# Kernel tuning notes

Measured on AMD Instinct MI355X. Metric: run time of the kernel, lower is better.

## Reference

```python
import jax, jax.numpy as jnp
import numpy as np

VOCAB = 50257
NUM_TAGS = 50
EMB_DIM = 128
CTX = 2
N_TOKENS = 262144


def setup_inputs() -> dict:
    key = jax.random.key(0)
    k1, k2, k3, k4 = jax.random.split(key, 4)
    tokens = jax.random.randint(k1, (N_TOKENS,), 0, VOCAB, dtype=jnp.int64 if jax.config.jax_enable_x64 else jnp.int32)
    emb_table = jax.random.normal(k2, (VOCAB, EMB_DIM), dtype=jnp.float32)
    W = jax.random.normal(k3, (NUM_TAGS, EMB_DIM * (1 + 2 * CTX)), dtype=jnp.float32) * 0.05
    b = jax.random.normal(k4, (NUM_TAGS,), dtype=jnp.float32) * 0.05
    return {"tokens": tokens, "emb_table": emb_table, "W": W, "b": b}


def reference(tokens, emb_table, W, b):
    # [N, D] embedding gather
    emb = emb_table[tokens]
    n = emb.shape[0]
    # zero-pad CTX positions on each side (matches torch.zeros_like padding)
    padded = jnp.pad(emb, ((CTX, CTX), (0, 0)))
    # sliding window concat: [N, (2*CTX+1)*D] via 2*CTX+1 shifted views
    windows = jnp.concatenate([padded[i:i + n] for i in range(2 * CTX + 1)], axis=-1)
    logits = windows @ W.T + b  # [N, num_tags]
    log_probs = jax.nn.log_softmax(logits, axis=-1)
    return log_probs
```

## Files before the change

### kernel.cpp

```cpp
#include <hip/hip_runtime.h>
#include <hip/hip_bf16.h>

#define VOCAB 50257
#define NTAGS 50
#define EMB   128
#define NTOK  262144
#define KD    640
#define WPAD  64

#define TPB   64
#define TOKPB 64
#define ROWS  68

typedef __attribute__((ext_vector_type(4))) float f32x4;
typedef __attribute__((ext_vector_type(8))) short bf16x8;

__device__ __forceinline__ ushort f2bf(float f) {
    union { float f; unsigned u; } v; v.f = f;
    unsigned u = v.u;
    return (ushort)((u + 0x7fffu + ((u >> 16) & 1u)) >> 16);
}

__device__ __forceinline__ void gload_lds16(const void* g, void* l) {
    __builtin_amdgcn_global_load_lds(
        (const __attribute__((address_space(1))) unsigned*)g,
        (__attribute__((address_space(3))) unsigned*)l, 16, 0, 0);
}

__global__ void conv_k(const float* __restrict__ emb, const float* __restrict__ W,
                       ushort* __restrict__ embb, ushort* __restrict__ wb) {
    const int etotal = (VOCAB + 1) * EMB;
    int idx = (blockIdx.x * blockDim.x + threadIdx.x) * 4;
    if (idx < etotal) {
        float4 v = {0.f, 0.f, 0.f, 0.f};
        if (idx < VOCAB * EMB) v = *(const float4*)(emb + idx);
        ushort4 o = { f2bf(v.x), f2bf(v.y), f2bf(v.z), f2bf(v.w) };
        *(ushort4*)(embb + idx) = o;
    } else {
        int wi = idx - etotal;
        if (wi < WPAD * KD) {
            #pragma unroll
            for (int k = 0; k < 4; ++k) {
                int j = wi + k;
                int tag = j / KD;
                wb[j] = f2bf(tag < NTAGS ? W[j] : 0.f);
            }
        }
    }
}

__global__ __launch_bounds__(TPB)
void tagger_k(const int* __restrict__ tokens, const ushort* __restrict__ embb,
              const ushort* __restrict__ Wb, const float* __restrict__ bias,
              float* __restrict__ out) {
    __shared__ ushort smem[ROWS * EMB];

    const int lane = threadIdx.x & 63;
    const int c = lane & 15;
    const int q = lane >> 4;
    const int bb = blockIdx.x * TOKPB;

    {
        const int rsub = lane >> 4;
        const int pc   = lane & 15;
        #pragma unroll
        for (int g = 0; g < 17; ++g) {
            int i = g * 4 + rsub;
            int t = bb - 2 + i;
            int tok = (t >= 0 && t < NTOK) ? tokens[t] : VOCAB;
            int sc = pc ^ (i & 7);
            gload_lds16(embb + (size_t)tok * EMB + sc * 8, (char*)smem + g * 1024);
        }
    }
    __syncthreads();

    f32x4 acc[4][4];
    #pragma unroll
    for (int mt = 0; mt < 4; ++mt)
        #pragma unroll
        for (int nt = 0; nt < 4; ++nt)
            acc[mt][nt] = (f32x4){0.f, 0.f, 0.f, 0.f};

    #pragma unroll
    for (int p = 0; p < 5; ++p) {
        #pragma unroll
        for (int kk = 0; kk < 4; ++kk) {
            bf16x8 a[4], bf[4];
            #pragma unroll
            for (int mt = 0; mt < 4; ++mt) {
                int r  = mt * 16 + c + p;
                int pc = (4 * kk + q) ^ (r & 7);
                a[mt] = *(const bf16x8*)((const char*)smem + r * 256 + pc * 16);
            }
            const int kf = p * 128 + kk * 32 + q * 8;
            #pragma unroll
            for (int nt = 0; nt < 4; ++nt)
                bf[nt] = *(const bf16x8*)(Wb + (nt * 16 + c) * KD + kf);
            __builtin_amdgcn_s_setprio(1);
            #pragma unroll
            for (int mt = 0; mt < 4; ++mt)
                #pragma unroll
                for (int nt = 0; nt < 4; ++nt)
                    acc[mt][nt] = __builtin_amdgcn_mfma_f32_16x16x32_bf16(
                        a[mt], bf[nt], acc[mt][nt], 0, 0, 0);
            __builtin_amdgcn_s_setprio(0);
        }
    }

    float bv[4];
    #pragma unroll
    for (int nt = 0; nt < 4; ++nt) {
        int tag = nt * 16 + c;
        bv[nt] = (tag < NTAGS) ? bias[tag] : 0.f;
    }

    #pragma unroll
    for (int mt = 0; mt < 4; ++mt) {
        #pragma unroll
        for (int j = 0; j < 4; ++j) {
            const int row = bb + mt * 16 + q * 4 + j;
            float v[4];
            float m = -1e30f;
            #pragma unroll
            for (int nt = 0; nt < 4; ++nt) {
                float x = acc[mt][nt][j] + bv[nt];
                v[nt] = x;
                if (nt * 16 + c < NTAGS) m = fmaxf(m, x);
            }
            #pragma unroll
            for (int mask = 8; mask >= 1; mask >>= 1)
                m = fmaxf(m, __shfl_xor(m, mask));
            float s = 0.f;
            #pragma unroll
            for (int nt = 0; nt < 4; ++nt)
                if (nt * 16 + c < NTAGS) s += __expf(v[nt] - m);
            #pragma unroll
            for (int mask = 8; mask >= 1; mask >>= 1)
                s += __shfl_xor(s, mask);
            const float L = m + __logf(s);
            #pragma unroll
            for (int nt = 0; nt < 4; ++nt) {
                int tag = nt * 16 + c;
                if (tag < NTAGS) out[row * NTAGS + tag] = v[nt] - L;
            }
        }
    }
}

extern "C" void kernel_launch(void* const* d_in, const int* in_sizes, int n_in,
                              void* d_out, int out_size, void* d_ws, size_t ws_size,
                              hipStream_t stream) {
    const int*   tokens = (const int*)d_in[0];
    const float* emb    = (const float*)d_in[1];
    const float* W      = (const float*)d_in[2];
    const float* b      = (const float*)d_in[3];
    float* out = (float*)d_out;

    ushort* embb = (ushort*)d_ws;
    ushort* Wb   = embb + (size_t)(VOCAB + 1) * EMB;

    {
        const int etotal = (VOCAB + 1) * EMB;
        const int total4 = (etotal + WPAD * KD) / 4;
        conv_k<<<(total4 + 255) / 256, 256, 0, stream>>>(emb, W, embb, Wb);
    }
    {
        const int nblk = NTOK / TOKPB;
        tagger_k<<<nblk, TPB, 0, stream>>>(tokens, embb, Wb, b, out);
    }
}
```

Baseline: 81.86 us.

## Software-pipeline MFMA loop with register prefetch of W and LDS fragments

Hoists the token index loads, the bias loads and the first W fragment loads ahead of the LDS gather. The k-loop becomes a flat 20-step loop with a 4-deep register ring for W fragments and a 2-deep ring for A fragments, so loads for later steps are issued while the current MFMAs run. Launch bounds now ask for 2 blocks per CU. The extra live registers raise VGPR pressure and could cause spills.

```diff
diff --git a/kernel.cpp b/kernel.cpp
--- a/kernel.cpp
+++ b/kernel.cpp
@@ -11,6 +11,7 @@
 #define TPB   64
 #define TOKPB 64
 #define ROWS  68
+#define STEPS 20
 
 typedef __attribute__((ext_vector_type(4))) float f32x4;
 typedef __attribute__((ext_vector_type(8))) short bf16x8;
@@ -49,7 +50,7 @@
     }
 }
 
-__global__ __launch_bounds__(TPB)
+__global__ __launch_bounds__(TPB, 2)
 void tagger_k(const int* __restrict__ tokens, const ushort* __restrict__ embb,
               const ushort* __restrict__ Wb, const float* __restrict__ bias,
               float* __restrict__ out) {
@@ -59,17 +60,41 @@
     const int c = lane & 15;
     const int q = lane >> 4;
     const int bb = blockIdx.x * TOKPB;
+    const int rsub = lane >> 4;
+
+    int tokid[17];
+    #pragma unroll
+    for (int g = 0; g < 17; ++g) {
+        int t = bb - 2 + g * 4 + rsub;
+        tokid[g] = (t >= 0 && t < NTOK) ? tokens[t] : VOCAB;
+    }
+
+    const ushort* bp[4];
+    #pragma unroll
+    for (int nt = 0; nt < 4; ++nt)
+        bp[nt] = Wb + (nt * 16 + c) * KD + q * 8;
+
+    bf16x8 Bb[4][4];
+    #pragma unroll
+    for (int s = 0; s < 4; ++s)
+        #pragma unroll
+        for (int nt = 0; nt < 4; ++nt)
+            Bb[s][nt] = *(const bf16x8*)(bp[nt] + (s >> 2) * 128 + (s & 3) * 32);
+
+    float bv[4];
+    #pragma unroll
+    for (int nt = 0; nt < 4; ++nt) {
+        int tag = nt * 16 + c;
+        bv[nt] = bias[tag < NTAGS ? tag : NTAGS - 1];
+    }
 
     {
-        const int rsub = lane >> 4;
-        const int pc   = lane & 15;
+        const int pc = lane & 15;
         #pragma unroll
         for (int g = 0; g < 17; ++g) {
             int i = g * 4 + rsub;
-            int t = bb - 2 + i;
-            int tok = (t >= 0 && t < NTOK) ? tokens[t] : VOCAB;
             int sc = pc ^ (i & 7);
-            gload_lds16(embb + (size_t)tok * EMB + sc * 8, (char*)smem + g * 1024);
+            gload_lds16(embb + (size_t)tokid[g] * EMB + sc * 8, (char*)smem + g * 1024);
         }
     }
     __syncthreads();
@@ -81,37 +106,43 @@
         for (int nt = 0; nt < 4; ++nt)
             acc[mt][nt] = (f32x4){0.f, 0.f, 0.f, 0.f};
 
-    #pragma unroll
-    for (int p = 0; p < 5; ++p) {
-        #pragma unroll
-        for (int kk = 0; kk < 4; ++kk) {
-            bf16x8 a[4], bf[4];
-            #pragma unroll
-            for (int mt = 0; mt < 4; ++mt) {
-                int r  = mt * 16 + c + p;
-                int pc = (4 * kk + q) ^ (r & 7);
-                a[mt] = *(const bf16x8*)((const char*)smem + r * 256 + pc * 16);
-            }
-            const int kf = p * 128 + kk * 32 + q * 8;
+    bf16x8 Ab[2][4];
+    #pragma unroll
+    for (int s = 0; s < 2; ++s) {
+        int p = s >> 2, kk = s & 3;
+        int h = (c + p) & 7;
+        int ch = (4 * kk + q) ^ h;
+        const char* ab = (const char*)smem + (c + p) * 256 + ch * 16;
+        #pragma unroll
+        for (int mt = 0; mt < 4; ++mt)
+            Ab[s][mt] = *(const bf16x8*)(ab + mt * 4096);
+    }
+
+    #pragma unroll
+    for (int s = 0; s < STEPS; ++s) {
+        __builtin_amdgcn_s_setprio(1);
+        #pragma unroll
+        for (int mt = 0; mt < 4; ++mt)
             #pragma unroll
             for (int nt = 0; nt < 4; ++nt)
-                bf[nt] = *(const bf16x8*)(Wb + (nt * 16 + c) * KD + kf);
-            __builtin_amdgcn_s_setprio(1);
+                acc[mt][nt] = __builtin_amdgcn_mfma_f32_16x16x32_bf16(
+                    Ab[s & 1][mt], Bb[s & 3][nt], acc[mt][nt], 0, 0, 0);
+        __builtin_amdgcn_s_setprio(0);
+        if (s + 4 < STEPS) {
+            const int t = s + 4, p = t >> 2, kk = t & 3;
+            #pragma unroll
+            for (int nt = 0; nt < 4; ++nt)
+                Bb[s & 3][nt] = *(const bf16x8*)(bp[nt] + p * 128 + kk * 32);
+        }
+        if (s + 2 < STEPS) {
+            const int t = s + 2, p = t >> 2, kk = t & 3;
+            int h = (c + p) & 7;
+            int ch = (4 * kk + q) ^ h;
+            const char* ab = (const char*)smem + (c + p) * 256 + ch * 16;
             #pragma unroll
             for (int mt = 0; mt < 4; ++mt)
-                #pragma unroll
-                for (int nt = 0; nt < 4; ++nt)
-                    acc[mt][nt] = __builtin_amdgcn_mfma_f32_16x16x32_bf16(
-                        a[mt], bf[nt], acc[mt][nt], 0, 0, 0);
-            __builtin_amdgcn_s_setprio(0);
-        }
-    }
-
-    float bv[4];
-    #pragma unroll
-    for (int nt = 0; nt < 4; ++nt) {
-        int tag = nt * 16 + c;
-        bv[nt] = (tag < NTAGS) ? bias[tag] : 0.f;
+                Ab[s & 1][mt] = *(const bf16x8*)(ab + mt * 4096);
+        }
     }
 
     #pragma unroll
```

New measurement: 74.19 us. 9.4% less time.
